# Kernel optimization log

Hardware: AMD Instinct MI355X
Metric: run time of the kernel (lower is better)

## Reference

```python
import jax, jax.numpy as jnp
import numpy as np

B, S, D = 1, 2048, 4096
H = 32
HD = D // H  # 128
THETA = 10000.0


def _precompute_freqs_cis(dim, end, dtype=jnp.float32):
    freqs = 1.0 / THETA ** (jnp.arange(0, dim, 2)[: dim // 2].astype(dtype) / dim)
    t = jnp.arange(end)
    freqs = jnp.outer(t, freqs).astype(dtype)
    return jnp.complex64(jnp.cos(freqs) + 1j * jnp.sin(freqs))  # [end, dim//2]


def _apply_rotary_emb(xq, xk, freqs_cis, dtype=jnp.float32):
    # xq, xk: [b, s, h, hd]; freqs_cis: [1, s, hd//2] complex
    rq = xq.astype(jnp.float32).reshape(*xq.shape[:-1], -1, 2)
    rk = xk.astype(jnp.float32).reshape(*xk.shape[:-1], -1, 2)
    xq_ = jax.lax.complex(rq[..., 0], rq[..., 1])
    xk_ = jax.lax.complex(rk[..., 0], rk[..., 1])
    fc = jnp.reshape(freqs_cis, (*freqs_cis.shape[:2], 1, *freqs_cis.shape[2:]))  # [1,s,1,hd//2]
    xq_out = xq_ * fc
    xk_out = xk_ * fc
    xq_out = jnp.stack((jnp.real(xq_out), jnp.imag(xq_out)), axis=-1).reshape(*xq_out.shape[:-1], -1)
    xk_out = jnp.stack((jnp.real(xk_out), jnp.imag(xk_out)), axis=-1).reshape(*xk_out.shape[:-1], -1)
    return xq_out.astype(dtype), xk_out.astype(dtype)


def setup_inputs() -> dict:
    key = jax.random.key(0)
    k1, k2, k3 = jax.random.split(key, 3)
    scale = 1.0 / np.sqrt(D)
    return {
        "hidden_states": jax.random.normal(k1, (B, S, D), dtype=jnp.float32),
        "w_qkv_kernel": jax.random.normal(k2, (D, 3 * D), dtype=jnp.float32) * scale,
        "wo_kernel": jax.random.normal(k3, (D, D), dtype=jnp.float32) * scale,
    }


def reference(hidden_states, w_qkv_kernel, wo_kernel):
    b, s, d = hidden_states.shape
    qkv = hidden_states @ w_qkv_kernel  # [b, s, 3d]
    q, k, v = jnp.split(qkv, 3, -1)
    q = q.reshape(b, s, H, HD)
    k = k.reshape(b, s, H, HD)
    v = v.reshape(b, s, H, HD)
    freq = _precompute_freqs_cis(HD, S)[:s].reshape(1, s, -1)
    q, k = _apply_rotary_emb(q, k, freq)
    attn = jnp.einsum("bqhd,bkhd->bhqk", q, k)
    attn = attn * (1.0 / np.sqrt(HD))
    attn = jax.nn.softmax(attn, axis=-1)
    out = jnp.einsum("bhqk,bkhd->bqhd", attn, v).reshape(b, s, d)
    return out @ wo_kernel
```

## Files before the change

### kernel.cpp

```cpp
#include <hip/hip_runtime.h>
#include <cstdint>

#define S_LEN   2048
#define D_MODEL 4096
#define NHEAD   32
#define HDIM    128
#define LDQKV   12288

typedef __bf16 bf16x8 __attribute__((ext_vector_type(8)));
typedef float  f32x4  __attribute__((ext_vector_type(4)));
typedef unsigned short u16;
typedef unsigned int   u32;

union U16x8 { u16 u[8]; uint4 v; };

static __device__ __forceinline__ u16 f2b(float f) {
  u32 u = __builtin_bit_cast(u32, f);
  u += 0x7fffu + ((u >> 16) & 1u);
  return (u16)(u >> 16);
}
static __device__ __forceinline__ float b2f(u16 h) {
  u32 u = ((u32)h) << 16;
  return __builtin_bit_cast(float, u);
}

#define GLOAD_LDS16(gp, lp)                                                   \
  __builtin_amdgcn_global_load_lds(                                           \
      (const __attribute__((address_space(1))) unsigned int*)(gp),            \
      (__attribute__((address_space(3))) unsigned int*)(lp), 16, 0, 0)

__global__ __launch_bounds__(256) void convert_f32_bf16(
    const float* __restrict__ in, u16* __restrict__ out) {
  size_t i = (size_t)blockIdx.x * 256 + threadIdx.x;
  const float4* p = (const float4*)in;
  float4 a = p[2 * i], b = p[2 * i + 1];
  U16x8 r;
  r.u[0] = f2b(a.x); r.u[1] = f2b(a.y); r.u[2] = f2b(a.z); r.u[3] = f2b(a.w);
  r.u[4] = f2b(b.x); r.u[5] = f2b(b.y); r.u[6] = f2b(b.z); r.u[7] = f2b(b.w);
  *(uint4*)(out + 8 * i) = r.v;
}

__global__ __launch_bounds__(256) void tconv(
    const float* __restrict__ in, u16* __restrict__ out, int R, int C) {
  __shared__ u16 tile[64][65];
  const int r0 = blockIdx.y * 64, c0 = blockIdx.x * 64;
  const int tid = threadIdx.x;
  const int tr = tid >> 4, tc = (tid & 15) * 4;
#pragma unroll
  for (int p = 0; p < 4; ++p) {
    float4 v = *(const float4*)(in + (size_t)(r0 + p * 16 + tr) * C + c0 + tc);
    u16* t = &tile[p * 16 + tr][tc];
    t[0] = f2b(v.x); t[1] = f2b(v.y); t[2] = f2b(v.z); t[3] = f2b(v.w);
  }
  __syncthreads();
  const int oc = tid >> 3, os = (tid & 7) * 8;
#pragma unroll
  for (int p = 0; p < 2; ++p) {
    U16x8 u;
#pragma unroll
    for (int j = 0; j < 8; ++j) u.u[j] = tile[os + j][p * 32 + oc];
    *(uint4*)(out + (size_t)(c0 + p * 32 + oc) * R + r0 + os) = u.v;
  }
}

template <typename OutT>
__global__ __launch_bounds__(256) void gemm_bt(
    const u16* __restrict__ A, const u16* __restrict__ Bt, OutT* __restrict__ C,
    int M, int N, int K) {
  __shared__ __align__(16) u16 As[128 * 64];
  __shared__ __align__(16) u16 Bs[128 * 64];
  const int tid = threadIdx.x;
  const int lane = tid & 63, wave = tid >> 6;
  const int lane15 = lane & 15, quad = lane >> 4;
  const int wm = (wave >> 1) * 64, wn = (wave & 1) * 64;
  const size_t bm = (size_t)blockIdx.y * 128, bn = (size_t)blockIdx.x * 128;
  const int sreg_row = lane >> 3;
  const int schunk = lane & 7;

  f32x4 acc[4][4] = {};

  for (int k0 = 0; k0 < K; k0 += 64) {
#pragma unroll
    for (int i = 0; i < 4; ++i) {
      const int reg = wave * 4 + i;
      const int row = reg * 8 + sreg_row;
      const int gc = schunk ^ (row & 7);
      GLOAD_LDS16(A + (bm + row) * (size_t)K + k0 + gc * 8, &As[reg * 512]);
      GLOAD_LDS16(Bt + (bn + row) * (size_t)K + k0 + gc * 8, &Bs[reg * 512]);
    }
    __syncthreads();
#pragma unroll
    for (int kk = 0; kk < 64; kk += 32) {
      const int cb = kk >> 3;
      bf16x8 af[4], bfr[4];
#pragma unroll
      for (int mt = 0; mt < 4; ++mt) {
        const int row = wm + mt * 16 + lane15;
        af[mt] = *(const bf16x8*)&As[row * 64 + (((cb + quad) ^ (lane15 & 7)) * 8)];
      }
#pragma unroll
      for (int nt = 0; nt < 4; ++nt) {
        const int row = wn + nt * 16 + lane15;
        bfr[nt] = *(const bf16x8*)&Bs[row * 64 + (((cb + quad) ^ (lane15 & 7)) * 8)];
      }
#pragma unroll
      for (int mt = 0; mt < 4; ++mt)
#pragma unroll
        for (int nt = 0; nt < 4; ++nt)
          acc[mt][nt] = __builtin_amdgcn_mfma_f32_16x16x32_bf16(
              af[mt], bfr[nt], acc[mt][nt], 0, 0, 0);
    }
    __syncthreads();
  }
#pragma unroll
  for (int mt = 0; mt < 4; ++mt)
#pragma unroll
    for (int r = 0; r < 4; ++r) {
      size_t row = bm + wm + mt * 16 + quad * 4 + r;
#pragma unroll
      for (int nt = 0; nt < 4; ++nt) {
        size_t col = bn + wn + nt * 16 + lane15;
        float v = acc[mt][nt][r];
        if constexpr (sizeof(OutT) == 2) C[row * N + col] = (OutT)f2b(v);
        else                             C[row * N + col] = v;
      }
    }
}

__global__ __launch_bounds__(256) void rope_kernel(u16* __restrict__ qkv) {
  int idx = blockIdx.x * 256 + threadIdx.x;
  int s = idx >> 11;
  int p = idx & 2047;
  int h = p >> 6, j = p & 63;
  float freq = exp2f(-(float)j * 0.20762050593046015f);
  float ang = (float)s * freq;
  float sn = __sinf(ang), cs = __cosf(ang);
  size_t base = (size_t)s * LDQKV + h * HDIM + 2 * j;
  u32 q = *(const u32*)(qkv + base);
  float q0 = b2f((u16)(q & 0xffff)), q1 = b2f((u16)(q >> 16));
  u32 qo = (u32)f2b(q0 * cs - q1 * sn) | ((u32)f2b(q0 * sn + q1 * cs) << 16);
  *(u32*)(qkv + base) = qo;
  u32 k = *(const u32*)(qkv + base + D_MODEL);
  float k0 = b2f((u16)(k & 0xffff)), k1 = b2f((u16)(k >> 16));
  u32 ko = (u32)f2b(k0 * cs - k1 * sn) | ((u32)f2b(k0 * sn + k1 * cs) << 16);
  *(u32*)(qkv + base + D_MODEL) = ko;
}

__global__ __launch_bounds__(256) void transpose_v(
    const u16* __restrict__ qkv, u16* __restrict__ vt) {
  __shared__ u16 tile[64][65];
  const int s0 = blockIdx.x * 64, d0 = blockIdx.y * 64, h = blockIdx.z;
  const int tid = threadIdx.x;
  const int tr = tid >> 3, tc = (tid & 7) * 8;
#pragma unroll
  for (int p = 0; p < 2; ++p) {
    U16x8 u;
    u.v = *(const uint4*)(qkv + (size_t)(s0 + p * 32 + tr) * LDQKV + 2 * D_MODEL +
                          h * HDIM + d0 + tc);
    u16* t = &tile[p * 32 + tr][tc];
#pragma unroll
    for (int j = 0; j < 8; ++j) t[j] = u.u[j];
  }
  __syncthreads();
  const int dd = tid >> 3, ss = (tid & 7) * 8;
#pragma unroll
  for (int p = 0; p < 2; ++p) {
    U16x8 u;
#pragma unroll
    for (int j = 0; j < 8; ++j) u.u[j] = tile[ss + j][p * 32 + dd];
    *(uint4*)(vt + (size_t)h * HDIM * S_LEN + (size_t)(d0 + p * 32 + dd) * S_LEN +
              s0 + ss) = u.v;
  }
}

__global__ __launch_bounds__(256, 2) void attn_kernel(
    const u16* __restrict__ qkv, const u16* __restrict__ vt, u16* __restrict__ ctx) {
  __shared__ __align__(16) u16 Ks[64 * 128];
  __shared__ __align__(16) u16 Vs[128 * 64];
  __shared__ __align__(16) u16 Ps[4][32 * 72];
  const int h = blockIdx.y, qt = blockIdx.x;
  const int tid = threadIdx.x;
  const int lane = tid & 63, wave = tid >> 6;
  const int lane15 = lane & 15, quad = lane >> 4;
  const int q0 = qt * 128 + wave * 32;

  bf16x8 aq[2][4];
#pragma unroll
  for (int mi = 0; mi < 2; ++mi)
#pragma unroll
    for (int kt = 0; kt < 4; ++kt)
      aq[mi][kt] = *(const bf16x8*)(qkv + (size_t)(q0 + mi * 16 + lane15) * LDQKV +
                                    h * HDIM + kt * 32 + quad * 8);

  f32x4 o[2][8] = {};
  float lsum[2][4] = {};

  const int krow_off = wave * 16 + (lane >> 4);
  const int kslot = lane & 15;
  const int vrow_off = wave * 32 + (lane >> 3);
  const int vslot = lane & 7;
  const u16* kbase = qkv + D_MODEL + h * HDIM;
  const u16* vbase = vt + (size_t)h * HDIM * S_LEN;
  const float cexp = 0.12751879523243985f;

  for (int kv0 = 0; kv0 < S_LEN; kv0 += 64) {
#pragma unroll
    for (int i = 0; i < 4; ++i) {
      const int krow = krow_off + i * 4;
      const int kgc = kslot ^ (krow & 7);
      GLOAD_LDS16(kbase + (size_t)(kv0 + krow) * LDQKV + kgc * 8,
                  &Ks[(wave * 16 + i * 4) * 128]);
      const int vrow = vrow_off + i * 8;
      const int vgc = vslot ^ (vrow & 7);
      GLOAD_LDS16(vbase + (size_t)vrow * S_LEN + kv0 + vgc * 8,
                  &Vs[(wave * 32 + i * 8) * 64]);
    }
    __syncthreads();

    f32x4 sf[2][4] = {};
#pragma unroll
    for (int nt = 0; nt < 4; ++nt) {
      bf16x8 bk[4];
#pragma unroll
      for (int kt = 0; kt < 4; ++kt)
        bk[kt] = *(const bf16x8*)&Ks[(nt * 16 + lane15) * 128 +
                                     (((kt * 4 + quad) ^ (lane15 & 7)) * 8)];
#pragma unroll
      for (int kt = 0; kt < 4; ++kt) {
        sf[0][nt] = __builtin_amdgcn_mfma_f32_16x16x32_bf16(aq[0][kt], bk[kt], sf[0][nt], 0, 0, 0);
        sf[1][nt] = __builtin_amdgcn_mfma_f32_16x16x32_bf16(aq[1][kt], bk[kt], sf[1][nt], 0, 0, 0);
      }
    }

#pragma unroll
    for (int mi = 0; mi < 2; ++mi)
#pragma unroll
      for (int nt = 0; nt < 4; ++nt)
#pragma unroll
        for (int r = 0; r < 4; ++r) {
          float pv = exp2f(sf[mi][nt][r] * cexp);
          lsum[mi][r] += pv;
          Ps[wave][(mi * 16 + quad * 4 + r) * 72 + nt * 16 + lane15] = f2b(pv);
        }

#pragma unroll
    for (int kt2 = 0; kt2 < 2; ++kt2) {
      bf16x8 ap0 = *(const bf16x8*)&Ps[wave][(lane15) * 72 + kt2 * 32 + quad * 8];
      bf16x8 ap1 = *(const bf16x8*)&Ps[wave][(16 + lane15) * 72 + kt2 * 32 + quad * 8];
#pragma unroll
      for (int nt2 = 0; nt2 < 8; ++nt2) {
        bf16x8 bv = *(const bf16x8*)&Vs[(nt2 * 16 + lane15) * 64 +
                                        (((kt2 * 4 + quad) ^ (lane15 & 7)) * 8)];
        o[0][nt2] = __builtin_amdgcn_mfma_f32_16x16x32_bf16(ap0, bv, o[0][nt2], 0, 0, 0);
        o[1][nt2] = __builtin_amdgcn_mfma_f32_16x16x32_bf16(ap1, bv, o[1][nt2], 0, 0, 0);
      }
    }
    __syncthreads();
  }

#pragma unroll
  for (int mi = 0; mi < 2; ++mi)
#pragma unroll
    for (int r = 0; r < 4; ++r) {
      float l = lsum[mi][r];
      l += __shfl_xor(l, 1);
      l += __shfl_xor(l, 2);
      l += __shfl_xor(l, 4);
      l += __shfl_xor(l, 8);
      float inv = 1.0f / l;
      size_t row = q0 + mi * 16 + quad * 4 + r;
#pragma unroll
      for (int nt2 = 0; nt2 < 8; ++nt2)
        ctx[row * D_MODEL + h * HDIM + nt2 * 16 + lane15] = f2b(o[mi][nt2][r] * inv);
    }
}

extern "C" void kernel_launch(void* const* d_in, const int* in_sizes, int n_in,
                              void* d_out, int out_size, void* d_ws, size_t ws_size,
                              hipStream_t stream) {
  const float* hs    = (const float*)d_in[0];
  const float* w_qkv = (const float*)d_in[1];
  const float* wo    = (const float*)d_in[2];
  float* out = (float*)d_out;

  char* w = (char*)d_ws;
  u16* hsb   = (u16*)(w);
  u16* wqkvT = (u16*)(w + (16u  << 20));
  u16* woT   = (u16*)(w + (112u << 20));
  u16* qkvb  = (u16*)(w + (144u << 20));
  u16* vt    = (u16*)(w + (192u << 20));
  u16* ctx   = hsb;

  convert_f32_bf16<<<4096, 256, 0, stream>>>(hs, hsb);
  tconv<<<dim3(12288 / 64, 4096 / 64), 256, 0, stream>>>(w_qkv, wqkvT, 4096, 12288);
  tconv<<<dim3(4096 / 64, 4096 / 64), 256, 0, stream>>>(wo, woT, 4096, 4096);

  gemm_bt<u16><<<dim3(12288 / 128, 2048 / 128), 256, 0, stream>>>(
      hsb, wqkvT, qkvb, 2048, 12288, 4096);

  rope_kernel<<<(S_LEN * 2048) / 256, 256, 0, stream>>>(qkvb);
  transpose_v<<<dim3(32, 2, 32), 256, 0, stream>>>(qkvb, vt);
  attn_kernel<<<dim3(16, 32), 256, 0, stream>>>(qkvb, vt, ctx);

  gemm_bt<float><<<dim3(4096 / 128, 2048 / 128), 256, 0, stream>>>(
      ctx, woT, out, 2048, 4096, 4096);
}
```

Measured before the change: 782.3 us.

## Register-prefetch next K/V tile during attention compute, raise MFMA priority

Swaps the direct global-to-LDS loads of each K/V tile for register staging. The next tile is loaded into registers right after the barrier, so its global latency overlaps the current tile's QK^T, softmax and PV work. The change also wraps the MFMA sections in s_setprio and uses the native exp2 builtin instead of exp2f. This costs extra VGPRs (8 uint4 per thread), which may lower occupancy, and it adds an explicit VGPR-to-LDS store step.

Result: slower. 914.3 us (+16.9%).

```diff
diff --git a/kernel.cpp b/kernel.cpp
--- a/kernel.cpp
+++ b/kernel.cpp
@@ -203,21 +203,40 @@
   const u16* vbase = vt + (size_t)h * HDIM * S_LEN;
   const float cexp = 0.12751879523243985f;
 
+  uint4 kreg[4], vreg[4];
+#pragma unroll
+  for (int i = 0; i < 4; ++i) {
+    const int krow = krow_off + i * 4;
+    const int kgc = kslot ^ (krow & 7);
+    kreg[i] = *(const uint4*)(kbase + (size_t)krow * LDQKV + kgc * 8);
+    const int vrow = vrow_off + i * 8;
+    const int vgc = vslot ^ (vrow & 7);
+    vreg[i] = *(const uint4*)(vbase + (size_t)vrow * S_LEN + vgc * 8);
+  }
+
   for (int kv0 = 0; kv0 < S_LEN; kv0 += 64) {
 #pragma unroll
     for (int i = 0; i < 4; ++i) {
-      const int krow = krow_off + i * 4;
-      const int kgc = kslot ^ (krow & 7);
-      GLOAD_LDS16(kbase + (size_t)(kv0 + krow) * LDQKV + kgc * 8,
-                  &Ks[(wave * 16 + i * 4) * 128]);
-      const int vrow = vrow_off + i * 8;
-      const int vgc = vslot ^ (vrow & 7);
-      GLOAD_LDS16(vbase + (size_t)vrow * S_LEN + kv0 + vgc * 8,
-                  &Vs[(wave * 32 + i * 8) * 64]);
+      *(uint4*)&Ks[(wave * 16 + i * 4) * 128 + lane * 8] = kreg[i];
+      *(uint4*)&Vs[(wave * 32 + i * 8) * 64 + lane * 8] = vreg[i];
     }
     __syncthreads();
 
+    if (kv0 + 64 < S_LEN) {
+      const int kv1 = kv0 + 64;
+#pragma unroll
+      for (int i = 0; i < 4; ++i) {
+        const int krow = krow_off + i * 4;
+        const int kgc = kslot ^ (krow & 7);
+        kreg[i] = *(const uint4*)(kbase + (size_t)(kv1 + krow) * LDQKV + kgc * 8);
+        const int vrow = vrow_off + i * 8;
+        const int vgc = vslot ^ (vrow & 7);
+        vreg[i] = *(const uint4*)(vbase + (size_t)vrow * S_LEN + kv1 + vgc * 8);
+      }
+    }
+
     f32x4 sf[2][4] = {};
+    __builtin_amdgcn_s_setprio(1);
 #pragma unroll
     for (int nt = 0; nt < 4; ++nt) {
       bf16x8 bk[4];
@@ -231,6 +250,7 @@
         sf[1][nt] = __builtin_amdgcn_mfma_f32_16x16x32_bf16(aq[1][kt], bk[kt], sf[1][nt], 0, 0, 0);
       }
     }
+    __builtin_amdgcn_s_setprio(0);
 
 #pragma unroll
     for (int mi = 0; mi < 2; ++mi)
@@ -238,11 +258,12 @@
       for (int nt = 0; nt < 4; ++nt)
 #pragma unroll
         for (int r = 0; r < 4; ++r) {
-          float pv = exp2f(sf[mi][nt][r] * cexp);
+          float pv = __builtin_amdgcn_exp2f(sf[mi][nt][r] * cexp);
           lsum[mi][r] += pv;
           Ps[wave][(mi * 16 + quad * 4 + r) * 72 + nt * 16 + lane15] = f2b(pv);
         }
 
+    __builtin_amdgcn_s_setprio(1);
 #pragma unroll
     for (int kt2 = 0; kt2 < 2; ++kt2) {
       bf16x8 ap0 = *(const bf16x8*)&Ps[wave][(lane15) * 72 + kt2 * 32 + quad * 8];
@@ -255,6 +276,7 @@
         o[1][nt2] = __builtin_amdgcn_mfma_f32_16x16x32_bf16(ap1, bv, o[1][nt2], 0, 0, 0);
       }
     }
+    __builtin_amdgcn_s_setprio(0);
     __syncthreads();
   }
 
```

## Replace GEMM with 256x256-tile double-buffered 8-wave pipelined kernel

Applied to the files above, without the earlier changes.

Replaces the 128x128 single-buffered 4-wave GEMM with a 256x256-tile, 8-wave (512-thread) kernel. Each K-step prefetches the next tile into a second LDS buffer while MFMAs run on the current one, interleaving fragment reads with MFMA phases and raising wave priority during MFMA. Workgroups are remapped across XCDs for L2 locality. It uses much more LDS (128KB) and registers, and launches far fewer workgroups (e.g. 128 for the output projection), which risks underfilling the GPU.

Measured after the change: 884.8 us. 13.1% more time.

```diff
diff --git a/kernel.cpp b/kernel.cpp
--- a/kernel.cpp
+++ b/kernel.cpp
@@ -64,67 +64,119 @@
 }
 
 template <typename OutT>
-__global__ __launch_bounds__(256) void gemm_bt(
+static __device__ __forceinline__ void gemm8p_body(
     const u16* __restrict__ A, const u16* __restrict__ Bt, OutT* __restrict__ C,
     int M, int N, int K) {
-  __shared__ __align__(16) u16 As[128 * 64];
-  __shared__ __align__(16) u16 Bs[128 * 64];
+  __shared__ __align__(16) u16 As[2][256 * 64];
+  __shared__ __align__(16) u16 Bs[2][256 * 64];
   const int tid = threadIdx.x;
   const int lane = tid & 63, wave = tid >> 6;
   const int lane15 = lane & 15, quad = lane >> 4;
-  const int wm = (wave >> 1) * 64, wn = (wave & 1) * 64;
-  const size_t bm = (size_t)blockIdx.y * 128, bn = (size_t)blockIdx.x * 128;
-  const int sreg_row = lane >> 3;
-  const int schunk = lane & 7;
-
-  f32x4 acc[4][4] = {};
-
-  for (int k0 = 0; k0 < K; k0 += 64) {
-#pragma unroll
-    for (int i = 0; i < 4; ++i) {
-      const int reg = wave * 4 + i;
-      const int row = reg * 8 + sreg_row;
-      const int gc = schunk ^ (row & 7);
-      GLOAD_LDS16(A + (bm + row) * (size_t)K + k0 + gc * 8, &As[reg * 512]);
-      GLOAD_LDS16(Bt + (bn + row) * (size_t)K + k0 + gc * 8, &Bs[reg * 512]);
-    }
-    __syncthreads();
-#pragma unroll
-    for (int kk = 0; kk < 64; kk += 32) {
-      const int cb = kk >> 3;
-      bf16x8 af[4], bfr[4];
-#pragma unroll
-      for (int mt = 0; mt < 4; ++mt) {
-        const int row = wm + mt * 16 + lane15;
-        af[mt] = *(const bf16x8*)&As[row * 64 + (((cb + quad) ^ (lane15 & 7)) * 8)];
-      }
-#pragma unroll
-      for (int nt = 0; nt < 4; ++nt) {
-        const int row = wn + nt * 16 + lane15;
-        bfr[nt] = *(const bf16x8*)&Bs[row * 64 + (((cb + quad) ^ (lane15 & 7)) * 8)];
-      }
-#pragma unroll
-      for (int mt = 0; mt < 4; ++mt)
-#pragma unroll
-        for (int nt = 0; nt < 4; ++nt)
-          acc[mt][nt] = __builtin_amdgcn_mfma_f32_16x16x32_bf16(
-              af[mt], bfr[nt], acc[mt][nt], 0, 0, 0);
-    }
-    __syncthreads();
-  }
-#pragma unroll
-  for (int mt = 0; mt < 4; ++mt)
+  const int wm = (wave >> 2) * 128, wn = (wave & 3) * 64;
+
+  const int nbx = gridDim.x;
+  const int nwg = nbx * gridDim.y;
+  const int lin = (int)blockIdx.y * nbx + (int)blockIdx.x;
+  const int xx = (lin & 7) * (nwg >> 3) + (lin >> 3);
+  const size_t bm = (size_t)(xx / nbx) * 256, bn = (size_t)(xx % nbx) * 256;
+
+  const int srow = wave * 8 + (lane >> 3);
+  const int scol = ((lane & 7) ^ (lane >> 3)) * 8;
+  const u16* pA = A + (bm + srow) * (size_t)K + scol;
+  const u16* pB = Bt + (bn + srow) * (size_t)K + scol;
+
+  f32x4 acc[8][4] = {};
+  bf16x8 af[4][2], bfr[2][2];
+
+#define STAGE8(buf, k0)                                                       \
+  {                                                                           \
+    _Pragma("unroll") for (int i = 0; i < 4; ++i) {                           \
+      GLOAD_LDS16(pA + (size_t)(i * 64) * K + (k0),                           \
+                  &As[buf][(i * 64 + wave * 8) * 64]);                        \
+      GLOAD_LDS16(pB + (size_t)(i * 64) * K + (k0),                           \
+                  &Bs[buf][(i * 64 + wave * 8) * 64]);                        \
+    }                                                                         \
+  }
+#define RDA8(buf, MB)                                                         \
+  _Pragma("unroll") for (int m = 0; m < 4; ++m)                               \
+      _Pragma("unroll") for (int kk = 0; kk < 2; ++kk)                        \
+          af[m][kk] = *(const bf16x8*)&As[buf][(wm + (MB + m) * 16 + lane15) * 64 + \
+                                              (((kk * 4 + quad) ^ (lane15 & 7)) * 8)];
+#define RDB8(buf, NB)                                                         \
+  _Pragma("unroll") for (int n = 0; n < 2; ++n)                               \
+      _Pragma("unroll") for (int kk = 0; kk < 2; ++kk)                        \
+          bfr[n][kk] = *(const bf16x8*)&Bs[buf][(wn + (NB + n) * 16 + lane15) * 64 + \
+                                               (((kk * 4 + quad) ^ (lane15 & 7)) * 8)];
+#define MM8(MB, NB)                                                           \
+  __builtin_amdgcn_s_setprio(1);                                              \
+  _Pragma("unroll") for (int m = 0; m < 4; ++m)                               \
+      _Pragma("unroll") for (int n = 0; n < 2; ++n)                           \
+          _Pragma("unroll") for (int kk = 0; kk < 2; ++kk)                    \
+              acc[MB + m][NB + n] = __builtin_amdgcn_mfma_f32_16x16x32_bf16(  \
+                  af[m][kk], bfr[n][kk], acc[MB + m][NB + n], 0, 0, 0);       \
+  __builtin_amdgcn_s_setprio(0);
+#define PHASE_PRE()                                                           \
+  __builtin_amdgcn_s_barrier();                                               \
+  __builtin_amdgcn_sched_barrier(0);
+#define KITER(CUR, T)                                                         \
+  {                                                                           \
+    RDA8(CUR, 0);                                                             \
+    RDB8(CUR, 0);                                                             \
+    if ((T) + 1 < nt) STAGE8(CUR ^ 1, ((T) + 1) << 6);                        \
+    PHASE_PRE(); MM8(0, 0); __builtin_amdgcn_s_barrier();                     \
+    RDB8(CUR, 2);                                                             \
+    PHASE_PRE(); MM8(0, 2); __builtin_amdgcn_s_barrier();                     \
+    RDA8(CUR, 4);                                                             \
+    PHASE_PRE(); MM8(4, 2); __builtin_amdgcn_s_barrier();                     \
+    RDB8(CUR, 0);                                                             \
+    PHASE_PRE(); MM8(4, 0);                                                   \
+    asm volatile("s_waitcnt vmcnt(0)" ::: "memory");                          \
+    __builtin_amdgcn_s_barrier();                                             \
+    __builtin_amdgcn_sched_barrier(0);                                        \
+  }
+
+  const int nt = K >> 6;
+  STAGE8(0, 0);
+  asm volatile("s_waitcnt vmcnt(0)" ::: "memory");
+  __builtin_amdgcn_s_barrier();
+
+  for (int t = 0; t < nt; t += 2) {
+    KITER(0, t);
+    KITER(1, t + 1);
+  }
+
+#undef STAGE8
+#undef RDA8
+#undef RDB8
+#undef MM8
+#undef PHASE_PRE
+#undef KITER
+
+#pragma unroll
+  for (int m = 0; m < 8; ++m)
 #pragma unroll
     for (int r = 0; r < 4; ++r) {
-      size_t row = bm + wm + mt * 16 + quad * 4 + r;
-#pragma unroll
-      for (int nt = 0; nt < 4; ++nt) {
-        size_t col = bn + wn + nt * 16 + lane15;
-        float v = acc[mt][nt][r];
+      size_t row = bm + wm + m * 16 + quad * 4 + r;
+#pragma unroll
+      for (int n = 0; n < 4; ++n) {
+        size_t col = bn + wn + n * 16 + lane15;
+        float v = acc[m][n][r];
         if constexpr (sizeof(OutT) == 2) C[row * N + col] = (OutT)f2b(v);
         else                             C[row * N + col] = v;
       }
     }
+}
+
+__global__ __launch_bounds__(512, 2) void gemm8p_qkv(
+    const u16* __restrict__ A, const u16* __restrict__ Bt, u16* __restrict__ C,
+    int M, int N, int K) {
+  gemm8p_body<u16>(A, Bt, C, M, N, K);
+}
+
+__global__ __launch_bounds__(512, 2) void gemm8p_out(
+    const u16* __restrict__ A, const u16* __restrict__ Bt, float* __restrict__ C,
+    int M, int N, int K) {
+  gemm8p_body<float>(A, Bt, C, M, N, K);
 }
 
 __global__ __launch_bounds__(256) void rope_kernel(u16* __restrict__ qkv) {
@@ -295,13 +347,13 @@
   tconv<<<dim3(12288 / 64, 4096 / 64), 256, 0, stream>>>(w_qkv, wqkvT, 4096, 12288);
   tconv<<<dim3(4096 / 64, 4096 / 64), 256, 0, stream>>>(wo, woT, 4096, 4096);
 
-  gemm_bt<u16><<<dim3(12288 / 128, 2048 / 128), 256, 0, stream>>>(
+  gemm8p_qkv<<<dim3(12288 / 256, 2048 / 256), 512, 0, stream>>>(
       hsb, wqkvT, qkvb, 2048, 12288, 4096);
 
   rope_kernel<<<(S_LEN * 2048) / 256, 256, 0, stream>>>(qkvb);
   transpose_v<<<dim3(32, 2, 32), 256, 0, stream>>>(qkvb, vt);
   attn_kernel<<<dim3(16, 32), 256, 0, stream>>>(qkvb, vt, ctx);
 
-  gemm_bt<float><<<dim3(4096 / 128, 2048 / 128), 256, 0, stream>>>(
+  gemm8p_out<<<dim3(4096 / 256, 2048 / 256), 512, 0, stream>>>(
       ctx, woT, out, 2048, 4096, 4096);
 }
```

## Replace QKV GEMM with 256x256 double-buffered direct-to-LDS pipelined kernel

Applied to the files above, without the earlier changes.

The QKV projection now uses a new 512-thread kernel with 256x256 output tiles. It double-buffers global-to-LDS loads with an XOR swizzle and interleaves explicit vmcnt waits and barriers with MFMA groups, raising wave priority during the MFMA groups. Workgroup indices are remapped across the grid, and the 12288-column GEMM is split into two 6144-column launches. This aims to raise data reuse and overlap loads with matrix math, at the cost of fewer workgroups per launch (192, below the CU count) and high LDS use that limits occupancy.

Result: slower. 825.3 us (+5.5%).

```diff
diff --git a/kernel.cpp b/kernel.cpp
--- a/kernel.cpp
+++ b/kernel.cpp
@@ -63,9 +63,136 @@
   }
 }
 
-template <typename OutT>
-__global__ __launch_bounds__(256) void gemm_bt(
-    const u16* __restrict__ A, const u16* __restrict__ Bt, OutT* __restrict__ C,
+#define SB0() __builtin_amdgcn_sched_barrier(0)
+#define SBAR() asm volatile("s_barrier" ::: "memory")
+#define VMW6() asm volatile("s_waitcnt vmcnt(6)" ::: "memory")
+#define VMW4() asm volatile("s_waitcnt vmcnt(4)" ::: "memory")
+#define VMW2() asm volatile("s_waitcnt vmcnt(2)" ::: "memory")
+#define VMW0() asm volatile("s_waitcnt vmcnt(0)" ::: "memory")
+#define BARF() SB0(); SBAR(); SB0()
+
+__global__ __launch_bounds__(512, 2) void gemm256v3_qkv(
+    const u16* __restrict__ A, const u16* __restrict__ Bt, u16* __restrict__ C,
+    int M, int NS, int K) {
+  __shared__ __align__(16) u16 As[2 * 16384];
+  __shared__ __align__(16) u16 Bs[2 * 16384];
+  const int tid = threadIdx.x;
+  const int lane = tid & 63, wave = tid >> 6;
+  const int lane15 = lane & 15, quad = lane >> 4;
+  const int g  = wave >> 2;
+  const int wg = wave & 3;
+  const int hB = (wave & 3) >> 1;
+  const int bb = (wave & 1) * 64;
+  const int wm = g * 128, wn = (wave & 3) * 64;
+  const int l8 = lane >> 3;
+  const int gcS = ((lane & 7) ^ l8) * 8;
+
+  const int nbx = gridDim.x;
+  const int nwg = nbx * gridDim.y;
+  const int lin = (int)blockIdx.y * nbx + (int)blockIdx.x;
+  const int xx = (lin & 7) * (nwg >> 3) + (lin >> 3);
+  const size_t bm = (size_t)(xx / nbx) * 256, bn = (size_t)(xx % nbx) * 256;
+
+  f32x4 acc[8][4] = {};
+  bf16x8 af[4][2], bfr[2][2], b0s[2][2];
+
+#define STG_A(buf, k0, r)                                                     \
+  GLOAD_LDS16(A + (size_t)(bm + g * 128 + (r) * 32 + wg * 8 + l8) * K + (k0) + gcS, \
+              &As[(buf) * 16384 + g * 8192 + ((r) * 32 + wg * 8) * 64])
+#define STG_B(buf, k0, r)                                                     \
+  GLOAD_LDS16(Bt + (size_t)(bn + wn + (r) * 16 + g * 8 + l8) * K + (k0) + gcS, \
+              &Bs[(buf) * 16384 + hB * 8192 + (bb + (r) * 16 + g * 8) * 64])
+#define RD_AF(buf, MB)                                                        \
+  _Pragma("unroll") for (int m = 0; m < 4; ++m)                               \
+      _Pragma("unroll") for (int kk = 0; kk < 2; ++kk)                        \
+          af[m][kk] = *(const bf16x8*)&As[(buf) * 16384 + g * 8192 +          \
+              (((MB) + m) * 16 + lane15) * 64 +                               \
+              (((kk * 4 + quad) ^ (lane15 & 7)) * 8)];
+#define RD_BF(buf, NB, DST)                                                   \
+  _Pragma("unroll") for (int n = 0; n < 2; ++n)                               \
+      _Pragma("unroll") for (int kk = 0; kk < 2; ++kk)                        \
+          DST[n][kk] = *(const bf16x8*)&Bs[(buf) * 16384 + hB * 8192 +        \
+              (bb + ((NB) + n) * 16 + lane15) * 64 +                          \
+              (((kk * 4 + quad) ^ (lane15 & 7)) * 8)];
+#define MFMA16(MB, NB, BOP)                                                   \
+  __builtin_amdgcn_s_setprio(1);                                              \
+  _Pragma("unroll") for (int m = 0; m < 4; ++m)                               \
+      _Pragma("unroll") for (int n = 0; n < 2; ++n)                           \
+          _Pragma("unroll") for (int kk = 0; kk < 2; ++kk)                    \
+              acc[(MB) + m][(NB) + n] = __builtin_amdgcn_mfma_f32_16x16x32_bf16( \
+                  af[m][kk], BOP[n][kk], acc[(MB) + m][(NB) + n], 0, 0, 0);   \
+  __builtin_amdgcn_s_setprio(0);
+
+  const int nt = K >> 6;
+  STG_B(0, 0, 0); STG_B(0, 0, 1);
+  STG_A(0, 0, 0); STG_A(0, 0, 1);
+  STG_B(0, 0, 2); STG_B(0, 0, 3);
+  STG_A(0, 0, 2); STG_A(0, 0, 3);
+  SB0(); VMW4(); BARF();
+
+  for (int t = 0; t < nt - 1; ++t) {
+    const int cur = t & 1, nxt = cur ^ 1;
+    const int kn = (t + 1) << 6;
+    RD_AF(cur, 0);
+    RD_BF(cur, 0, b0s);
+    STG_B(nxt, kn, 0); STG_B(nxt, kn, 1);
+    STG_A(nxt, kn, 0); STG_A(nxt, kn, 1);
+    SB0(); VMW6(); BARF();
+    MFMA16(0, 0, b0s);
+    BARF();
+    RD_BF(cur, 2, bfr);
+    STG_B(nxt, kn, 2); STG_B(nxt, kn, 3);
+    SB0(); VMW6(); BARF();
+    MFMA16(0, 2, bfr);
+    BARF();
+    RD_AF(cur, 4);
+    STG_A(nxt, kn, 2); STG_A(nxt, kn, 3);
+    BARF();
+    MFMA16(4, 2, bfr);
+    BARF();
+    SB0(); VMW4(); BARF();
+    MFMA16(4, 0, b0s);
+    BARF();
+  }
+  {
+    const int cur = (nt - 1) & 1;
+    RD_AF(cur, 0);
+    RD_BF(cur, 0, b0s);
+    SB0(); VMW2(); BARF();
+    MFMA16(0, 0, b0s);
+    BARF();
+    RD_BF(cur, 2, bfr);
+    SB0(); VMW0(); BARF();
+    MFMA16(0, 2, bfr);
+    BARF();
+    RD_AF(cur, 4);
+    BARF();
+    MFMA16(4, 2, bfr);
+    BARF();
+    MFMA16(4, 0, b0s);
+  }
+
+#undef STG_A
+#undef STG_B
+#undef RD_AF
+#undef RD_BF
+#undef MFMA16
+
+#pragma unroll
+  for (int m = 0; m < 8; ++m)
+#pragma unroll
+    for (int r = 0; r < 4; ++r) {
+      size_t row = bm + wm + m * 16 + quad * 4 + r;
+#pragma unroll
+      for (int n = 0; n < 4; ++n) {
+        size_t col = bn + wn + n * 16 + lane15;
+        C[row * NS + col] = f2b(acc[m][n][r]);
+      }
+    }
+}
+
+__global__ __launch_bounds__(256) void gemm_bt_out(
+    const u16* __restrict__ A, const u16* __restrict__ Bt, float* __restrict__ C,
     int M, int N, int K) {
   __shared__ __align__(16) u16 As[128 * 64];
   __shared__ __align__(16) u16 Bs[128 * 64];
@@ -120,9 +247,7 @@
 #pragma unroll
       for (int nt = 0; nt < 4; ++nt) {
         size_t col = bn + wn + nt * 16 + lane15;
-        float v = acc[mt][nt][r];
-        if constexpr (sizeof(OutT) == 2) C[row * N + col] = (OutT)f2b(v);
-        else                             C[row * N + col] = v;
+        C[row * N + col] = acc[mt][nt][r];
       }
     }
 }
@@ -295,13 +420,15 @@
   tconv<<<dim3(12288 / 64, 4096 / 64), 256, 0, stream>>>(w_qkv, wqkvT, 4096, 12288);
   tconv<<<dim3(4096 / 64, 4096 / 64), 256, 0, stream>>>(wo, woT, 4096, 4096);
 
-  gemm_bt<u16><<<dim3(12288 / 128, 2048 / 128), 256, 0, stream>>>(
+  gemm256v3_qkv<<<dim3(24, 8), 512, 0, stream>>>(
       hsb, wqkvT, qkvb, 2048, 12288, 4096);
+  gemm256v3_qkv<<<dim3(24, 8), 512, 0, stream>>>(
+      hsb, wqkvT + (size_t)6144 * 4096, qkvb + 6144, 2048, 12288, 4096);
 
   rope_kernel<<<(S_LEN * 2048) / 256, 256, 0, stream>>>(qkvb);
   transpose_v<<<dim3(32, 2, 32), 256, 0, stream>>>(qkvb, vt);
   attn_kernel<<<dim3(16, 32), 256, 0, stream>>>(qkvb, vt, ctx);
 
-  gemm_bt<float><<<dim3(4096 / 128, 2048 / 128), 256, 0, stream>>>(
+  gemm_bt_out<<<dim3(4096 / 128, 2048 / 128), 256, 0, stream>>>(
       ctx, woT, out, 2048, 4096, 4096);
 }
```
